# Kernel tuning notes

Measured on AMD Instinct MI355X. Metric: run time of the kernel, lower is better.

## Reference

```python
import jax, jax.numpy as jnp
import numpy as np

F = 18      # n_frames (hard-coded by norm_scale vectors in the original)
P = 1024    # n_partitions
E = 2048    # n_hidden == n_features
H = 8       # n_head
HD = E // H
C = 64      # n_cluster


def setup_inputs() -> dict:
    key = jax.random.key(0)
    ks = jax.random.split(key, 11)
    s = 0.02
    return {
        "emb": jax.random.normal(ks[0], (F, P, E), jnp.float32),
        "Wq": jax.random.normal(ks[1], (E, E), jnp.float32) * s,
        "Wk": jax.random.normal(ks[2], (E, E), jnp.float32) * s,
        "Wv": jax.random.normal(ks[3], (E, E), jnp.float32) * s,
        "bq": jax.random.normal(ks[4], (E,), jnp.float32) * s,
        "bk": jax.random.normal(ks[5], (E,), jnp.float32) * s,
        "bv": jax.random.normal(ks[6], (E,), jnp.float32) * s,
        "Wo": jax.random.normal(ks[7], (E, E), jnp.float32) * s,
        "bo": jax.random.normal(ks[8], (E,), jnp.float32) * s,
        "Wmp": jax.random.normal(ks[9], (C, E), jnp.float32) * s,
        "bmp": jax.random.normal(ks[10], (C,), jnp.float32) * s,
    }


def reference(emb, Wq, Wk, Wv, bq, bk, bv, Wo, bo, Wmp, bmp):
    # message_passing path of CRF_SelfAttention (eval mode, dropout off).
    # The original folds each window's frames into the batch dim
    # (cat(chunk(group2, scale, 0), 1)), so MultiheadAttention runs with
    # sequence length 1: each token attends only to itself.
    x = emb.reshape(F * P, E)                        # tokens
    q = (x @ Wq.T + bq).reshape(-1, H, HD)
    k = (x @ Wk.T + bk).reshape(-1, H, HD)
    v = (x @ Wv.T + bv).reshape(-1, H, HD)
    scores = jnp.einsum('nhd,nhd->nh', q, k) / jnp.sqrt(jnp.float32(HD))
    attn = jax.nn.softmax(scores[..., None], axis=-1)  # [N,H,1] -> all ones
    ctx = attn * v                                     # [N,H,HD]
    Y = (ctx.reshape(-1, E) @ Wo.T + bo).reshape(F, P, E)

    # Per scale, frame t is covered by counts_s[t] identical window outputs
    # (the hard-coded norm_scale vectors); accumulate then divide.
    # NOTE: the original uses multihead_attn_scale2 for ALL scales.
    t = jnp.arange(F)
    gaccum = jnp.zeros_like(Y)
    for scale in (2, 4, 6):
        counts = jnp.minimum(jnp.minimum(t + 1, scale),
                             jnp.minimum(F - t, F - scale + 1)).astype(Y.dtype)
        gval = Y * counts[:, None, None]
        gaccum = gaccum + gval / counts[:, None, None]
    pairwise = 0.25 * gaccum                          # [F,P,E]
    pairwise = pairwise.transpose(1, 0, 2)            # [P,F,E]
    return pairwise @ Wmp.T + bmp                     # [P,F,C]
```

## Files before the change

### kernel.cpp

```cpp
#include <hip/hip_runtime.h>
#include <hip/hip_bf16.h>
#include <stdint.h>

typedef __bf16 bf16_t;
typedef __bf16 bf16x8 __attribute__((ext_vector_type(8)));
typedef __bf16 bf16x4 __attribute__((ext_vector_type(4)));
typedef float f32x4 __attribute__((ext_vector_type(4)));
typedef float f32x4v __attribute__((ext_vector_type(4)));

#define Edim 2048
#define Cdim 64
#define Fdim 18
#define Pdim 1024
#define Ntok (Fdim * Pdim)
#define KSPLIT 16

__device__ __forceinline__ bf16x8 cvt8(const float* __restrict__ p) {
    float4 lo = *(const float4*)p;
    float4 hi = *(const float4*)(p + 4);
    bf16x8 r;
    r[0] = (bf16_t)lo.x; r[1] = (bf16_t)lo.y; r[2] = (bf16_t)lo.z; r[3] = (bf16_t)lo.w;
    r[4] = (bf16_t)hi.x; r[5] = (bf16_t)hi.y; r[6] = (bf16_t)hi.z; r[7] = (bf16_t)hi.w;
    return r;
}

__device__ __forceinline__ bf16x8 cvt8_nt(const float* __restrict__ p) {
    f32x4v lo = __builtin_nontemporal_load((const f32x4v*)p);
    f32x4v hi = __builtin_nontemporal_load((const f32x4v*)p + 1);
    bf16x8 r;
    r[0] = (bf16_t)lo[0]; r[1] = (bf16_t)lo[1]; r[2] = (bf16_t)lo[2]; r[3] = (bf16_t)lo[3];
    r[4] = (bf16_t)hi[0]; r[5] = (bf16_t)hi[1]; r[6] = (bf16_t)hi[2]; r[7] = (bf16_t)hi[3];
    return r;
}

template <bool A_IS_F32>
__global__ __launch_bounds__(256) void splitk_gemm_kernel(
    const void* __restrict__ Am, const float* __restrict__ Bm,
    float* __restrict__ parts)
{
    const int tid  = threadIdx.x;
    const int wave = tid >> 6;
    const int lane = tid & 63;
    const int l15  = lane & 15;
    const int koct = lane >> 4;
    const int n0   = blockIdx.x * 64;
    const int kb   = blockIdx.y * 128;

    f32x4 acc[4] = {};

    #pragma unroll
    for (int i = 0; i < 4; ++i) {
        const int k0 = kb + i * 32;
        bf16x8 a;
        if constexpr (A_IS_F32)
            a = cvt8((const float*)Am + (size_t)(wave * 16 + l15) * Edim + k0 + koct * 8);
        else
            a = *(const bf16x8*)((const bf16_t*)Am + (size_t)(wave * 16 + l15) * Edim + k0 + koct * 8);
        #pragma unroll
        for (int t = 0; t < 4; ++t) {
            const float* src = Bm + (size_t)(k0 + koct * 8) * Edim + n0 + t * 16 + l15;
            bf16x8 b;
            #pragma unroll
            for (int j = 0; j < 8; ++j) b[j] = (bf16_t)src[(size_t)j * Edim];
            acc[t] = __builtin_amdgcn_mfma_f32_16x16x32_bf16(a, b, acc[t], 0, 0, 0);
        }
    }

    float* dst = parts + (size_t)blockIdx.y * (Cdim * Edim);
    #pragma unroll
    for (int t = 0; t < 4; ++t) {
        #pragma unroll
        for (int r = 0; r < 4; ++r) {
            int m = wave * 16 + koct * 4 + r;
            int n = n0 + t * 16 + l15;
            dst[(size_t)m * Edim + n] = acc[t][r];
        }
    }
}

__global__ __launch_bounds__(256) void reduce_bias_kernel(
    const float* __restrict__ parts, const float* __restrict__ Wmp,
    const float* __restrict__ bv, const float* __restrict__ bo,
    const float* __restrict__ bmp,
    bf16_t* __restrict__ A_bf, float* __restrict__ beff)
{
    const int c   = blockIdx.x;
    const int tid = threadIdx.x;
    const int col = tid * 8;

    float4 s0 = {0.f, 0.f, 0.f, 0.f}, s1 = {0.f, 0.f, 0.f, 0.f};
    #pragma unroll
    for (int j = 0; j < KSPLIT; ++j) {
        const float* p = parts + (size_t)j * (Cdim * Edim) + (size_t)c * Edim + col;
        float4 v0 = *(const float4*)p;
        float4 v1 = *(const float4*)(p + 4);
        s0.x += v0.x; s0.y += v0.y; s0.z += v0.z; s0.w += v0.w;
        s1.x += v1.x; s1.y += v1.y; s1.z += v1.z; s1.w += v1.w;
    }

    bf16x8 r;
    r[0] = (bf16_t)s0.x; r[1] = (bf16_t)s0.y; r[2] = (bf16_t)s0.z; r[3] = (bf16_t)s0.w;
    r[4] = (bf16_t)s1.x; r[5] = (bf16_t)s1.y; r[6] = (bf16_t)s1.z; r[7] = (bf16_t)s1.w;
    *(bf16x8*)(A_bf + (size_t)c * Edim + col) = r;

    float4 b0 = *(const float4*)(bv + col);
    float4 b1 = *(const float4*)(bv + col + 4);
    float4 w0 = *(const float4*)(Wmp + (size_t)c * Edim + col);
    float4 w1 = *(const float4*)(Wmp + (size_t)c * Edim + col + 4);
    float4 o0 = *(const float4*)(bo + col);
    float4 o1 = *(const float4*)(bo + col + 4);

    float s = s0.x * b0.x + s0.y * b0.y + s0.z * b0.z + s0.w * b0.w
            + s1.x * b1.x + s1.y * b1.y + s1.z * b1.z + s1.w * b1.w
            + w0.x * o0.x + w0.y * o0.y + w0.z * o0.z + w0.w * o0.w
            + w1.x * o1.x + w1.y * o1.y + w1.z * o1.z + w1.w * o1.w;

    #pragma unroll
    for (int off = 32; off > 0; off >>= 1) s += __shfl_down(s, off);

    __shared__ float red[4];
    if ((tid & 63) == 0) red[tid >> 6] = s;
    __syncthreads();
    if (tid == 0)
        beff[c] = 0.75f * (red[0] + red[1] + red[2] + red[3]) + bmp[c];
}

__global__ __launch_bounds__(256) void reduce_parts_kernel(
    const float* __restrict__ parts, bf16_t* __restrict__ out, float scale)
{
    const int idx = (blockIdx.x * 256 + threadIdx.x) * 4;
    float4 s = {0.f, 0.f, 0.f, 0.f};
    #pragma unroll
    for (int j = 0; j < KSPLIT; ++j) {
        float4 v = *(const float4*)(parts + (size_t)j * (Cdim * Edim) + idx);
        s.x += v.x; s.y += v.y; s.z += v.z; s.w += v.w;
    }
    bf16x4 r;
    r[0] = (bf16_t)(scale * s.x); r[1] = (bf16_t)(scale * s.y);
    r[2] = (bf16_t)(scale * s.z); r[3] = (bf16_t)(scale * s.w);
    *(bf16x4*)(out + idx) = r;
}

__global__ __launch_bounds__(256, 2) void main_gemm_kernel(
    const float* __restrict__ X, const bf16_t* __restrict__ Weff,
    const float* __restrict__ b_eff, float* __restrict__ out)
{
    __shared__ float red[4 * 64 * 33];

    const int tid  = threadIdx.x;
    const int wave = tid >> 6;
    const int lane = tid & 63;
    const int l15  = lane & 15;
    const int koct = lane >> 4;

    const int rbase = blockIdx.x * 32;
    const float* x0 = X + (size_t)(rbase + l15) * Edim;
    const float* x1 = x0 + (size_t)16 * Edim;
    const int kbase = wave * 512;

    f32x4 acc[2][4] = {};

    #pragma unroll 8
    for (int k0 = kbase; k0 < kbase + 512; k0 += 32) {
        bf16x8 a0 = cvt8_nt(x0 + k0 + koct * 8);
        bf16x8 a1 = cvt8_nt(x1 + k0 + koct * 8);
        #pragma unroll
        for (int t = 0; t < 4; ++t) {
            bf16x8 b = *(const bf16x8*)(Weff + (size_t)(t * 16 + l15) * Edim + k0 + koct * 8);
            acc[0][t] = __builtin_amdgcn_mfma_f32_16x16x32_bf16(a0, b, acc[0][t], 0, 0, 0);
            acc[1][t] = __builtin_amdgcn_mfma_f32_16x16x32_bf16(a1, b, acc[1][t], 0, 0, 0);
        }
    }

    {
        float* dst = &red[wave * 2112 + lane * 33];
        #pragma unroll
        for (int e = 0; e < 2; ++e)
            #pragma unroll
            for (int t = 0; t < 4; ++t)
                #pragma unroll
                for (int r = 0; r < 4; ++r) dst[e * 16 + t * 4 + r] = acc[e][t][r];
    }
    __syncthreads();

    {
        const int c  = wave * 16 + l15;
        const float be = b_eff[c];
        #pragma unroll
        for (int e = 0; e < 2; ++e) {
            #pragma unroll
            for (int r = 0; r < 4; ++r) {
                float v = 0.f;
                #pragma unroll
                for (int ws = 0; ws < 4; ++ws)
                    v += red[ws * 2112 + lane * 33 + e * 16 + wave * 4 + r];
                const int m = rbase + e * 16 + koct * 4 + r;
                const int f = m >> 10;
                const int p = m & 1023;
                out[(size_t)(p * Fdim + f) * Cdim + c] = v + be;
            }
        }
    }
}

extern "C" void kernel_launch(void* const* d_in, const int* in_sizes, int n_in,
                              void* d_out, int out_size, void* d_ws, size_t ws_size,
                              hipStream_t stream)
{
    const float* emb = (const float*)d_in[0];
    const float* Wv  = (const float*)d_in[3];
    const float* bv  = (const float*)d_in[6];
    const float* Wo  = (const float*)d_in[7];
    const float* bo  = (const float*)d_in[8];
    const float* Wmp = (const float*)d_in[9];
    const float* bmp = (const float*)d_in[10];

    const size_t PART = (size_t)Cdim * Edim;
    float*  parts1 = (float*)d_ws;
    float*  parts2 = parts1 + (size_t)KSPLIT * PART;
    bf16_t* A_bf   = (bf16_t*)(parts2 + (size_t)KSPLIT * PART);
    bf16_t* Weffb  = A_bf + PART;
    float*  beff   = (float*)(Weffb + PART);

    float* out = (float*)d_out;

    splitk_gemm_kernel<true><<<dim3(32, KSPLIT), 256, 0, stream>>>(Wmp, Wo, parts1);
    reduce_bias_kernel<<<64, 256, 0, stream>>>(parts1, Wmp, bv, bo, bmp, A_bf, beff);
    splitk_gemm_kernel<false><<<dim3(32, KSPLIT), 256, 0, stream>>>(A_bf, Wv, parts2);
    reduce_parts_kernel<<<128, 256, 0, stream>>>(parts2, Weffb, 0.75f);
    main_gemm_kernel<<<Ntok / 32, 256, 0, stream>>>(emb, Weffb, beff, out);
}
```

Baseline: 299.6 us.

## Fuse all stages into one persistent kernel with software grid barriers

Replaces the five separate launches with one persistent kernel of 512 blocks that runs the split-K weight GEMMs, their reductions and the main GEMM back to back. Stages are separated by atomic-counter grid barriers, and the bias reductions now use atomics into a zeroed buffer. The main GEMM becomes a grid-stride loop over 576 tiles, so work is uneven across blocks. It also drops the nontemporal loads and lowers the unroll from 8 to 4. The aim is to remove launch gaps and the tail of each stage, at the cost of barrier spin time, a memset launch, and relying on all 512 blocks being resident at once.

New measurement: 501.8 us. 67.5% more time.

```diff
diff --git a/kernel.cpp b/kernel.cpp
--- a/kernel.cpp
+++ b/kernel.cpp
@@ -4,9 +4,7 @@
 
 typedef __bf16 bf16_t;
 typedef __bf16 bf16x8 __attribute__((ext_vector_type(8)));
-typedef __bf16 bf16x4 __attribute__((ext_vector_type(4)));
 typedef float f32x4 __attribute__((ext_vector_type(4)));
-typedef float f32x4v __attribute__((ext_vector_type(4)));
 
 #define Edim 2048
 #define Cdim 64
@@ -14,6 +12,7 @@
 #define Pdim 1024
 #define Ntok (Fdim * Pdim)
 #define KSPLIT 16
+#define NBLK 512
 
 __device__ __forceinline__ bf16x8 cvt8(const float* __restrict__ p) {
     float4 lo = *(const float4*)p;
@@ -24,28 +23,25 @@
     return r;
 }
 
-__device__ __forceinline__ bf16x8 cvt8_nt(const float* __restrict__ p) {
-    f32x4v lo = __builtin_nontemporal_load((const f32x4v*)p);
-    f32x4v hi = __builtin_nontemporal_load((const f32x4v*)p + 1);
-    bf16x8 r;
-    r[0] = (bf16_t)lo[0]; r[1] = (bf16_t)lo[1]; r[2] = (bf16_t)lo[2]; r[3] = (bf16_t)lo[3];
-    r[4] = (bf16_t)hi[0]; r[5] = (bf16_t)hi[1]; r[6] = (bf16_t)hi[2]; r[7] = (bf16_t)hi[3];
-    return r;
+__device__ __forceinline__ void gridbar(int* cnt, int phase) {
+    __syncthreads();
+    if (threadIdx.x == 0) {
+        __threadfence();
+        atomicAdd(&cnt[phase], 1);
+        while (__hip_atomic_load(&cnt[phase], __ATOMIC_RELAXED,
+                                 __HIP_MEMORY_SCOPE_AGENT) < NBLK)
+            __builtin_amdgcn_s_sleep(8);
+        __threadfence();
+    }
+    __syncthreads();
 }
 
 template <bool A_IS_F32>
-__global__ __launch_bounds__(256) void splitk_gemm_kernel(
+__device__ __forceinline__ void splitk_body(
     const void* __restrict__ Am, const float* __restrict__ Bm,
-    float* __restrict__ parts)
+    float* __restrict__ dst, int n0, int kb,
+    int wave, int l15, int koct)
 {
-    const int tid  = threadIdx.x;
-    const int wave = tid >> 6;
-    const int lane = tid & 63;
-    const int l15  = lane & 15;
-    const int koct = lane >> 4;
-    const int n0   = blockIdx.x * 64;
-    const int kb   = blockIdx.y * 128;
-
     f32x4 acc[4] = {};
 
     #pragma unroll
@@ -66,7 +62,6 @@
         }
     }
 
-    float* dst = parts + (size_t)blockIdx.y * (Cdim * Edim);
     #pragma unroll
     for (int t = 0; t < 4; ++t) {
         #pragma unroll
@@ -78,126 +73,119 @@
     }
 }
 
-__global__ __launch_bounds__(256) void reduce_bias_kernel(
-    const float* __restrict__ parts, const float* __restrict__ Wmp,
-    const float* __restrict__ bv, const float* __restrict__ bo,
-    const float* __restrict__ bmp,
-    bf16_t* __restrict__ A_bf, float* __restrict__ beff)
-{
-    const int c   = blockIdx.x;
-    const int tid = threadIdx.x;
-    const int col = tid * 8;
-
-    float4 s0 = {0.f, 0.f, 0.f, 0.f}, s1 = {0.f, 0.f, 0.f, 0.f};
-    #pragma unroll
-    for (int j = 0; j < KSPLIT; ++j) {
-        const float* p = parts + (size_t)j * (Cdim * Edim) + (size_t)c * Edim + col;
-        float4 v0 = *(const float4*)p;
-        float4 v1 = *(const float4*)(p + 4);
-        s0.x += v0.x; s0.y += v0.y; s0.z += v0.z; s0.w += v0.w;
-        s1.x += v1.x; s1.y += v1.y; s1.z += v1.z; s1.w += v1.w;
-    }
-
-    bf16x8 r;
-    r[0] = (bf16_t)s0.x; r[1] = (bf16_t)s0.y; r[2] = (bf16_t)s0.z; r[3] = (bf16_t)s0.w;
-    r[4] = (bf16_t)s1.x; r[5] = (bf16_t)s1.y; r[6] = (bf16_t)s1.z; r[7] = (bf16_t)s1.w;
-    *(bf16x8*)(A_bf + (size_t)c * Edim + col) = r;
-
-    float4 b0 = *(const float4*)(bv + col);
-    float4 b1 = *(const float4*)(bv + col + 4);
-    float4 w0 = *(const float4*)(Wmp + (size_t)c * Edim + col);
-    float4 w1 = *(const float4*)(Wmp + (size_t)c * Edim + col + 4);
-    float4 o0 = *(const float4*)(bo + col);
-    float4 o1 = *(const float4*)(bo + col + 4);
-
-    float s = s0.x * b0.x + s0.y * b0.y + s0.z * b0.z + s0.w * b0.w
-            + s1.x * b1.x + s1.y * b1.y + s1.z * b1.z + s1.w * b1.w
-            + w0.x * o0.x + w0.y * o0.y + w0.z * o0.z + w0.w * o0.w
-            + w1.x * o1.x + w1.y * o1.y + w1.z * o1.z + w1.w * o1.w;
-
-    #pragma unroll
-    for (int off = 32; off > 0; off >>= 1) s += __shfl_down(s, off);
-
-    __shared__ float red[4];
-    if ((tid & 63) == 0) red[tid >> 6] = s;
-    __syncthreads();
-    if (tid == 0)
-        beff[c] = 0.75f * (red[0] + red[1] + red[2] + red[3]) + bmp[c];
-}
-
-__global__ __launch_bounds__(256) void reduce_parts_kernel(
-    const float* __restrict__ parts, bf16_t* __restrict__ out, float scale)
-{
-    const int idx = (blockIdx.x * 256 + threadIdx.x) * 4;
-    float4 s = {0.f, 0.f, 0.f, 0.f};
-    #pragma unroll
-    for (int j = 0; j < KSPLIT; ++j) {
-        float4 v = *(const float4*)(parts + (size_t)j * (Cdim * Edim) + idx);
-        s.x += v.x; s.y += v.y; s.z += v.z; s.w += v.w;
-    }
-    bf16x4 r;
-    r[0] = (bf16_t)(scale * s.x); r[1] = (bf16_t)(scale * s.y);
-    r[2] = (bf16_t)(scale * s.z); r[3] = (bf16_t)(scale * s.w);
-    *(bf16x4*)(out + idx) = r;
-}
-
-__global__ __launch_bounds__(256, 2) void main_gemm_kernel(
-    const float* __restrict__ X, const bf16_t* __restrict__ Weff,
-    const float* __restrict__ b_eff, float* __restrict__ out)
+__global__ __launch_bounds__(256, 2) void fused_kernel(
+    const float* __restrict__ X,
+    const float* __restrict__ Wv,  const float* __restrict__ bv,
+    const float* __restrict__ Wo,  const float* __restrict__ bo,
+    const float* __restrict__ Wmp, const float* __restrict__ bmp,
+    int* __restrict__ cnt, float* __restrict__ beff,
+    float* __restrict__ parts1, float* __restrict__ parts2,
+    bf16_t* __restrict__ A_bf, bf16_t* __restrict__ Weffb,
+    float* __restrict__ out)
 {
     __shared__ float red[4 * 64 * 33];
 
+    const int b    = blockIdx.x;
     const int tid  = threadIdx.x;
     const int wave = tid >> 6;
     const int lane = tid & 63;
     const int l15  = lane & 15;
     const int koct = lane >> 4;
 
-    const int rbase = blockIdx.x * 32;
-    const float* x0 = X + (size_t)(rbase + l15) * Edim;
-    const float* x1 = x0 + (size_t)16 * Edim;
-    const int kbase = wave * 512;
-
-    f32x4 acc[2][4] = {};
-
-    #pragma unroll 8
-    for (int k0 = kbase; k0 < kbase + 512; k0 += 32) {
-        bf16x8 a0 = cvt8_nt(x0 + k0 + koct * 8);
-        bf16x8 a1 = cvt8_nt(x1 + k0 + koct * 8);
-        #pragma unroll
-        for (int t = 0; t < 4; ++t) {
-            bf16x8 b = *(const bf16x8*)(Weff + (size_t)(t * 16 + l15) * Edim + k0 + koct * 8);
-            acc[0][t] = __builtin_amdgcn_mfma_f32_16x16x32_bf16(a0, b, acc[0][t], 0, 0, 0);
-            acc[1][t] = __builtin_amdgcn_mfma_f32_16x16x32_bf16(a1, b, acc[1][t], 0, 0, 0);
-        }
-    }
-
-    {
-        float* dst = &red[wave * 2112 + lane * 33];
-        #pragma unroll
-        for (int e = 0; e < 2; ++e)
-            #pragma unroll
-            for (int t = 0; t < 4; ++t)
+    {
+        const int n0 = (b & 31) * 64;
+        const int kb = (b >> 5) * 128;
+        splitk_body<true>(Wmp, Wo, parts1 + (size_t)(b >> 5) * (Cdim * Edim),
+                          n0, kb, wave, l15, koct);
+    }
+    gridbar(cnt, 0);
+
+    {
+        const int c    = b >> 3;
+        const int col0 = (b & 7) * 256;
+        const int col  = col0 + tid;
+
+        float a = 0.f;
+        #pragma unroll
+        for (int j = 0; j < KSPLIT; ++j)
+            a += parts1[(size_t)j * (Cdim * Edim) + (size_t)c * Edim + col];
+
+        A_bf[(size_t)c * Edim + col] = (bf16_t)a;
+
+        float s = a * bv[col] + Wmp[(size_t)c * Edim + col] * bo[col];
+        #pragma unroll
+        for (int off = 32; off > 0; off >>= 1) s += __shfl_down(s, off);
+        if (lane == 0) atomicAdd(&beff[c], 0.75f * s);
+        if ((b & 7) == 0 && tid == 0) atomicAdd(&beff[c], bmp[c]);
+    }
+    gridbar(cnt, 1);
+
+    {
+        const int n0 = (b & 31) * 64;
+        const int kb = (b >> 5) * 128;
+        splitk_body<false>(A_bf, Wv, parts2 + (size_t)(b >> 5) * (Cdim * Edim),
+                           n0, kb, wave, l15, koct);
+    }
+    gridbar(cnt, 2);
+
+    {
+        const int i = b * 256 + tid;
+        float s = 0.f;
+        #pragma unroll
+        for (int j = 0; j < KSPLIT; ++j)
+            s += parts2[(size_t)j * (Cdim * Edim) + i];
+        Weffb[i] = (bf16_t)(0.75f * s);
+    }
+    gridbar(cnt, 3);
+
+    for (int tile = b; tile < Ntok / 32; tile += NBLK) {
+        const int rbase = tile * 32;
+        const float* x0 = X + (size_t)(rbase + l15) * Edim;
+        const float* x1 = x0 + (size_t)16 * Edim;
+        const int kbase = wave * 512;
+
+        f32x4 acc[2][4] = {};
+
+        #pragma unroll 4
+        for (int k0 = kbase; k0 < kbase + 512; k0 += 32) {
+            bf16x8 a0 = cvt8(x0 + k0 + koct * 8);
+            bf16x8 a1 = cvt8(x1 + k0 + koct * 8);
+            #pragma unroll
+            for (int t = 0; t < 4; ++t) {
+                bf16x8 bfr = *(const bf16x8*)(Weffb + (size_t)(t * 16 + l15) * Edim + k0 + koct * 8);
+                acc[0][t] = __builtin_amdgcn_mfma_f32_16x16x32_bf16(a0, bfr, acc[0][t], 0, 0, 0);
+                acc[1][t] = __builtin_amdgcn_mfma_f32_16x16x32_bf16(a1, bfr, acc[1][t], 0, 0, 0);
+            }
+        }
+
+        __syncthreads();
+        {
+            float* dst = &red[wave * 2112 + lane * 33];
+            #pragma unroll
+            for (int e = 0; e < 2; ++e)
                 #pragma unroll
-                for (int r = 0; r < 4; ++r) dst[e * 16 + t * 4 + r] = acc[e][t][r];
-    }
-    __syncthreads();
-
-    {
-        const int c  = wave * 16 + l15;
-        const float be = b_eff[c];
-        #pragma unroll
-        for (int e = 0; e < 2; ++e) {
-            #pragma unroll
-            for (int r = 0; r < 4; ++r) {
-                float v = 0.f;
+                for (int t = 0; t < 4; ++t)
+                    #pragma unroll
+                    for (int r = 0; r < 4; ++r) dst[e * 16 + t * 4 + r] = acc[e][t][r];
+        }
+        __syncthreads();
+
+        {
+            const int c  = wave * 16 + l15;
+            const float be = beff[c];
+            #pragma unroll
+            for (int e = 0; e < 2; ++e) {
                 #pragma unroll
-                for (int ws = 0; ws < 4; ++ws)
-                    v += red[ws * 2112 + lane * 33 + e * 16 + wave * 4 + r];
-                const int m = rbase + e * 16 + koct * 4 + r;
-                const int f = m >> 10;
-                const int p = m & 1023;
-                out[(size_t)(p * Fdim + f) * Cdim + c] = v + be;
+                for (int r = 0; r < 4; ++r) {
+                    float v = 0.f;
+                    #pragma unroll
+                    for (int ws = 0; ws < 4; ++ws)
+                        v += red[ws * 2112 + lane * 33 + e * 16 + wave * 4 + r];
+                    const int m = rbase + e * 16 + koct * 4 + r;
+                    const int f = m >> 10;
+                    const int p = m & 1023;
+                    out[(size_t)(p * Fdim + f) * Cdim + c] = v + be;
+                }
             }
         }
     }
@@ -216,17 +204,19 @@
     const float* bmp = (const float*)d_in[10];
 
     const size_t PART = (size_t)Cdim * Edim;
-    float*  parts1 = (float*)d_ws;
+    uint8_t* base  = (uint8_t*)d_ws;
+    int*    cnt    = (int*)base;
+    float*  beff   = (float*)(base + 64);
+    float*  parts1 = (float*)(base + 1024);
     float*  parts2 = parts1 + (size_t)KSPLIT * PART;
     bf16_t* A_bf   = (bf16_t*)(parts2 + (size_t)KSPLIT * PART);
     bf16_t* Weffb  = A_bf + PART;
-    float*  beff   = (float*)(Weffb + PART);
 
     float* out = (float*)d_out;
 
-    splitk_gemm_kernel<true><<<dim3(32, KSPLIT), 256, 0, stream>>>(Wmp, Wo, parts1);
-    reduce_bias_kernel<<<64, 256, 0, stream>>>(parts1, Wmp, bv, bo, bmp, A_bf, beff);
-    splitk_gemm_kernel<false><<<dim3(32, KSPLIT), 256, 0, stream>>>(A_bf, Wv, parts2);
-    reduce_parts_kernel<<<128, 256, 0, stream>>>(parts2, Weffb, 0.75f);
-    main_gemm_kernel<<<Ntok / 32, 256, 0, stream>>>(emb, Weffb, beff, out);
-}
+    hipMemsetAsync(base, 0, 1024, stream);
+
+    fused_kernel<<<NBLK, 256, 0, stream>>>(
+        emb, Wv, bv, Wo, bo, Wmp, bmp,
+        cnt, beff, parts1, parts2, A_bf, Weffb, out);
+}
```

## Halve main GEMM row tile, raise occupancy, software-prefetch X loads

Applied to the files above, without the earlier changes.

Cuts the main GEMM block tile from 32 to 16 token rows, so twice as many blocks are launched and the shared reduction buffer shrinks. Launch bounds now ask for 4 blocks per CU instead of 2. X rows are prefetched one k-step ahead in registers, replacing the nontemporal loads with ordinary loads. The aim is more memory-level parallelism on the bandwidth-bound fp32 read of emb, at the cost of loading the Weff tiles twice as often.

Result: no change. 304.1 us (+1.5%).

```diff
diff --git a/kernel.cpp b/kernel.cpp
--- a/kernel.cpp
+++ b/kernel.cpp
@@ -6,7 +6,6 @@
 typedef __bf16 bf16x8 __attribute__((ext_vector_type(8)));
 typedef __bf16 bf16x4 __attribute__((ext_vector_type(4)));
 typedef float f32x4 __attribute__((ext_vector_type(4)));
-typedef float f32x4v __attribute__((ext_vector_type(4)));
 
 #define Edim 2048
 #define Cdim 64
@@ -24,9 +23,7 @@
     return r;
 }
 
-__device__ __forceinline__ bf16x8 cvt8_nt(const float* __restrict__ p) {
-    f32x4v lo = __builtin_nontemporal_load((const f32x4v*)p);
-    f32x4v hi = __builtin_nontemporal_load((const f32x4v*)p + 1);
+__device__ __forceinline__ bf16x8 cvt8r(f32x4 lo, f32x4 hi) {
     bf16x8 r;
     r[0] = (bf16_t)lo[0]; r[1] = (bf16_t)lo[1]; r[2] = (bf16_t)lo[2]; r[3] = (bf16_t)lo[3];
     r[4] = (bf16_t)hi[0]; r[5] = (bf16_t)hi[1]; r[6] = (bf16_t)hi[2]; r[7] = (bf16_t)hi[3];
@@ -141,11 +138,11 @@
     *(bf16x4*)(out + idx) = r;
 }
 
-__global__ __launch_bounds__(256, 2) void main_gemm_kernel(
+__global__ __launch_bounds__(256, 4) void main_gemm_kernel(
     const float* __restrict__ X, const bf16_t* __restrict__ Weff,
     const float* __restrict__ b_eff, float* __restrict__ out)
 {
-    __shared__ float red[4 * 64 * 33];
+    __shared__ float red[4 * 64 * 17];
 
     const int tid  = threadIdx.x;
     const int wave = tid >> 6;
@@ -153,33 +150,44 @@
     const int l15  = lane & 15;
     const int koct = lane >> 4;
 
-    const int rbase = blockIdx.x * 32;
-    const float* x0 = X + (size_t)(rbase + l15) * Edim;
-    const float* x1 = x0 + (size_t)16 * Edim;
+    const int rbase = blockIdx.x * 16;
+    const float* xp = X + (size_t)(rbase + l15) * Edim + koct * 8;
     const int kbase = wave * 512;
 
-    f32x4 acc[2][4] = {};
-
-    #pragma unroll 8
-    for (int k0 = kbase; k0 < kbase + 512; k0 += 32) {
-        bf16x8 a0 = cvt8_nt(x0 + k0 + koct * 8);
-        bf16x8 a1 = cvt8_nt(x1 + k0 + koct * 8);
+    f32x4 acc[4] = {};
+
+    f32x4 pa = *(const f32x4*)(xp + kbase);
+    f32x4 pb = *(const f32x4*)(xp + kbase + 4);
+
+    #pragma unroll 5
+    for (int i = 0; i < 15; ++i) {
+        const int k0 = kbase + i * 32;
+        f32x4 na = *(const f32x4*)(xp + k0 + 32);
+        f32x4 nb = *(const f32x4*)(xp + k0 + 36);
+        bf16x8 a = cvt8r(pa, pb);
         #pragma unroll
         for (int t = 0; t < 4; ++t) {
             bf16x8 b = *(const bf16x8*)(Weff + (size_t)(t * 16 + l15) * Edim + k0 + koct * 8);
-            acc[0][t] = __builtin_amdgcn_mfma_f32_16x16x32_bf16(a0, b, acc[0][t], 0, 0, 0);
-            acc[1][t] = __builtin_amdgcn_mfma_f32_16x16x32_bf16(a1, b, acc[1][t], 0, 0, 0);
-        }
-    }
-
+            acc[t] = __builtin_amdgcn_mfma_f32_16x16x32_bf16(a, b, acc[t], 0, 0, 0);
+        }
+        pa = na; pb = nb;
+    }
     {
-        float* dst = &red[wave * 2112 + lane * 33];
-        #pragma unroll
-        for (int e = 0; e < 2; ++e)
+        const int k0 = kbase + 480;
+        bf16x8 a = cvt8r(pa, pb);
+        #pragma unroll
+        for (int t = 0; t < 4; ++t) {
+            bf16x8 b = *(const bf16x8*)(Weff + (size_t)(t * 16 + l15) * Edim + k0 + koct * 8);
+            acc[t] = __builtin_amdgcn_mfma_f32_16x16x32_bf16(a, b, acc[t], 0, 0, 0);
+        }
+    }
+
+    {
+        float* dst = &red[wave * 1088 + lane * 17];
+        #pragma unroll
+        for (int t = 0; t < 4; ++t)
             #pragma unroll
-            for (int t = 0; t < 4; ++t)
-                #pragma unroll
-                for (int r = 0; r < 4; ++r) dst[e * 16 + t * 4 + r] = acc[e][t][r];
+            for (int r = 0; r < 4; ++r) dst[t * 4 + r] = acc[t][r];
     }
     __syncthreads();
 
@@ -187,18 +195,15 @@
         const int c  = wave * 16 + l15;
         const float be = b_eff[c];
         #pragma unroll
-        for (int e = 0; e < 2; ++e) {
+        for (int r = 0; r < 4; ++r) {
+            float v = 0.f;
             #pragma unroll
-            for (int r = 0; r < 4; ++r) {
-                float v = 0.f;
-                #pragma unroll
-                for (int ws = 0; ws < 4; ++ws)
-                    v += red[ws * 2112 + lane * 33 + e * 16 + wave * 4 + r];
-                const int m = rbase + e * 16 + koct * 4 + r;
-                const int f = m >> 10;
-                const int p = m & 1023;
-                out[(size_t)(p * Fdim + f) * Cdim + c] = v + be;
-            }
+            for (int ws = 0; ws < 4; ++ws)
+                v += red[ws * 1088 + lane * 17 + wave * 4 + r];
+            const int m = rbase + koct * 4 + r;
+            const int f = m >> 10;
+            const int p = m & 1023;
+            out[(size_t)(p * Fdim + f) * Cdim + c] = v + be;
         }
     }
 }
@@ -228,5 +233,5 @@
     reduce_bias_kernel<<<64, 256, 0, stream>>>(parts1, Wmp, bv, bo, bmp, A_bf, beff);
     splitk_gemm_kernel<false><<<dim3(32, KSPLIT), 256, 0, stream>>>(A_bf, Wv, parts2);
     reduce_parts_kernel<<<128, 256, 0, stream>>>(parts2, Weffb, 0.75f);
-    main_gemm_kernel<<<Ntok / 32, 256, 0, stream>>>(emb, Weffb, beff, out);
-}
+    main_gemm_kernel<<<Ntok / 16, 256, 0, stream>>>(emb, Weffb, beff, out);
+}
```

## Stage X tiles in LDS via global_load_lds and split waves over N

Applied to the files above, without the earlier changes.

The main GEMM now copies each 32×256 fp32 tile of the activations into LDS with direct global-to-LDS loads. Each wave then computes its own 16 output columns over the full K, rather than a K-slice for all columns. This removes the cross-wave LDS reduction and its large shared buffer. In exchange it adds a barrier per K-chunk with no double buffering, so load latency is not overlapped with MFMA work.

Result: faster. 290.2 us (-3.1%).

```diff
diff --git a/kernel.cpp b/kernel.cpp
--- a/kernel.cpp
+++ b/kernel.cpp
@@ -6,7 +6,6 @@
 typedef __bf16 bf16x8 __attribute__((ext_vector_type(8)));
 typedef __bf16 bf16x4 __attribute__((ext_vector_type(4)));
 typedef float f32x4 __attribute__((ext_vector_type(4)));
-typedef float f32x4v __attribute__((ext_vector_type(4)));
 
 #define Edim 2048
 #define Cdim 64
@@ -14,6 +13,11 @@
 #define Pdim 1024
 #define Ntok (Fdim * Pdim)
 #define KSPLIT 16
+
+#define BM 32
+#define BK 256
+#define NCHUNK (Edim / BK)
+#define XSTRIDE 260
 
 __device__ __forceinline__ bf16x8 cvt8(const float* __restrict__ p) {
     float4 lo = *(const float4*)p;
@@ -24,9 +28,7 @@
     return r;
 }
 
-__device__ __forceinline__ bf16x8 cvt8_nt(const float* __restrict__ p) {
-    f32x4v lo = __builtin_nontemporal_load((const f32x4v*)p);
-    f32x4v hi = __builtin_nontemporal_load((const f32x4v*)p + 1);
+__device__ __forceinline__ bf16x8 cvt8r(f32x4 lo, f32x4 hi) {
     bf16x8 r;
     r[0] = (bf16_t)lo[0]; r[1] = (bf16_t)lo[1]; r[2] = (bf16_t)lo[2]; r[3] = (bf16_t)lo[3];
     r[4] = (bf16_t)hi[0]; r[5] = (bf16_t)hi[1]; r[6] = (bf16_t)hi[2]; r[7] = (bf16_t)hi[3];
@@ -145,7 +147,7 @@
     const float* __restrict__ X, const bf16_t* __restrict__ Weff,
     const float* __restrict__ b_eff, float* __restrict__ out)
 {
-    __shared__ float red[4 * 64 * 33];
+    __shared__ __align__(16) float xs[BM * XSTRIDE];
 
     const int tid  = threadIdx.x;
     const int wave = tid >> 6;
@@ -153,52 +155,48 @@
     const int l15  = lane & 15;
     const int koct = lane >> 4;
 
-    const int rbase = blockIdx.x * 32;
-    const float* x0 = X + (size_t)(rbase + l15) * Edim;
-    const float* x1 = x0 + (size_t)16 * Edim;
-    const int kbase = wave * 512;
-
-    f32x4 acc[2][4] = {};
-
-    #pragma unroll 8
-    for (int k0 = kbase; k0 < kbase + 512; k0 += 32) {
-        bf16x8 a0 = cvt8_nt(x0 + k0 + koct * 8);
-        bf16x8 a1 = cvt8_nt(x1 + k0 + koct * 8);
-        #pragma unroll
-        for (int t = 0; t < 4; ++t) {
-            bf16x8 b = *(const bf16x8*)(Weff + (size_t)(t * 16 + l15) * Edim + k0 + koct * 8);
-            acc[0][t] = __builtin_amdgcn_mfma_f32_16x16x32_bf16(a0, b, acc[0][t], 0, 0, 0);
-            acc[1][t] = __builtin_amdgcn_mfma_f32_16x16x32_bf16(a1, b, acc[1][t], 0, 0, 0);
-        }
-    }
-
-    {
-        float* dst = &red[wave * 2112 + lane * 33];
-        #pragma unroll
-        for (int e = 0; e < 2; ++e)
-            #pragma unroll
-            for (int t = 0; t < 4; ++t)
-                #pragma unroll
-                for (int r = 0; r < 4; ++r) dst[e * 16 + t * 4 + r] = acc[e][t][r];
-    }
-    __syncthreads();
-
-    {
-        const int c  = wave * 16 + l15;
-        const float be = b_eff[c];
-        #pragma unroll
-        for (int e = 0; e < 2; ++e) {
-            #pragma unroll
-            for (int r = 0; r < 4; ++r) {
-                float v = 0.f;
-                #pragma unroll
-                for (int ws = 0; ws < 4; ++ws)
-                    v += red[ws * 2112 + lane * 33 + e * 16 + wave * 4 + r];
-                const int m = rbase + e * 16 + koct * 4 + r;
-                const int f = m >> 10;
-                const int p = m & 1023;
-                out[(size_t)(p * Fdim + f) * Cdim + c] = v + be;
-            }
+    const int rbase = blockIdx.x * BM;
+    const int c     = wave * 16 + l15;
+    const bf16_t* wrow = Weff + (size_t)c * Edim;
+
+    f32x4 acc0 = {}, acc1 = {};
+
+    for (int kc = 0; kc < NCHUNK; ++kc) {
+        if (kc) __syncthreads();
+
+        #pragma unroll
+        for (int i = 0; i < 8; ++i) {
+            const int r = wave * 8 + i;
+            const float* gsrc = X + (size_t)(rbase + r) * Edim + kc * BK + lane * 4;
+            __builtin_amdgcn_global_load_lds(
+                (const __attribute__((address_space(1))) void*)gsrc,
+                (__attribute__((address_space(3))) void*)&xs[r * XSTRIDE],
+                16, 0, 0);
+        }
+        __syncthreads();
+
+        #pragma unroll
+        for (int ks = 0; ks < BK; ks += 32) {
+            const float* a0p = &xs[l15 * XSTRIDE + ks + koct * 8];
+            const float* a1p = a0p + 16 * XSTRIDE;
+            bf16x8 a0 = cvt8r(*(const f32x4*)a0p, *(const f32x4*)(a0p + 4));
+            bf16x8 a1 = cvt8r(*(const f32x4*)a1p, *(const f32x4*)(a1p + 4));
+            bf16x8 b  = *(const bf16x8*)(wrow + kc * BK + ks + koct * 8);
+            acc0 = __builtin_amdgcn_mfma_f32_16x16x32_bf16(a0, b, acc0, 0, 0, 0);
+            acc1 = __builtin_amdgcn_mfma_f32_16x16x32_bf16(a1, b, acc1, 0, 0, 0);
+        }
+    }
+
+    const float be = b_eff[c];
+    #pragma unroll
+    for (int e = 0; e < 2; ++e) {
+        f32x4 a = e ? acc1 : acc0;
+        #pragma unroll
+        for (int r = 0; r < 4; ++r) {
+            const int m = rbase + e * 16 + koct * 4 + r;
+            const int f = m >> 10;
+            const int p = m & 1023;
+            out[(size_t)(p * Fdim + f) * Cdim + c] = a[r] + be;
         }
     }
 }
@@ -228,5 +226,5 @@
     reduce_bias_kernel<<<64, 256, 0, stream>>>(parts1, Wmp, bv, bo, bmp, A_bf, beff);
     splitk_gemm_kernel<false><<<dim3(32, KSPLIT), 256, 0, stream>>>(A_bf, Wv, parts2);
     reduce_parts_kernel<<<128, 256, 0, stream>>>(parts2, Weffb, 0.75f);
-    main_gemm_kernel<<<Ntok / 32, 256, 0, stream>>>(emb, Weffb, beff, out);
-}
+    main_gemm_kernel<<<Ntok / BM, 256, 0, stream>>>(emb, Weffb, beff, out);
+}
```
